# Performance work log

Measured on AMD Instinct MI355X. Metric: run time of the kernel, lower is better.

Reference implementation:

```python
import jax, jax.numpy as jnp
import numpy as np

G = 8          # grid_size
N = G * G      # 64 nodes
DEG = 17       # neighbors per node for 8x8 sudoku (2x4 boxes)
STEPS = 32
H = 96         # hidden_dim
E = 16         # embed_size
B = 16         # batch


def sudoku_edges():
    # row (7) + col (7) + 2x4 box (7) neighbors, set-union -> 17 per node
    idx = np.arange(N).reshape(G, G)
    nb = []
    for j in range(N):
        r, c = j // G, j % G
        br, bc = (r // 2) * 2, (c // 4) * 4
        s = set(idx[r, :].tolist()) | set(idx[:, c].tolist()) | set(idx[br:br + 2, bc:bc + 4].flatten().tolist())
        s.discard(j)
        nb.append(sorted(s))
    return np.asarray(nb, dtype=np.int32)  # [64, 17]


def setup_inputs() -> dict:
    key = jax.random.key(0)
    ks = jax.random.split(key, 16)
    sc = 0.05
    inp = {
        "x": jax.random.randint(ks[0], (B, G, G), 0, G + 1),            # given digits, 0 = blank
        "target": jax.random.randint(ks[1], (B, G, G), 0, G) + 1,       # solutions in 1..8
        "edges": jnp.asarray(sudoku_edges()),                            # [64, 17] int32
        "digit_emb": jax.random.normal(ks[2], (G + 1, E), jnp.float32) * sc,
        "row_emb": jax.random.normal(ks[3], (G, E), jnp.float32) * sc,
        "col_emb": jax.random.normal(ks[4], (G, E), jnp.float32) * sc,
        "in0_W": jax.random.normal(ks[5], (3 * E, H), jnp.float32) * sc,
        "in0_b": jnp.zeros((H,), jnp.float32),
        "in_Ws": jax.random.normal(ks[6], (3, H, H), jnp.float32) * sc,
        "in_bs": jnp.zeros((3, H), jnp.float32),
        "msg0_W": jax.random.normal(ks[7], (2 * H, H), jnp.float32) * sc,
        "msg0_b": jnp.zeros((H,), jnp.float32),
        "msg_Ws": jax.random.normal(ks[8], (3, H, H), jnp.float32) * sc,
        "msg_bs": jnp.zeros((3, H), jnp.float32),
        "W_ih": jax.random.normal(ks[9], (2 * H, 4 * H), jnp.float32) * sc,
        "W_hh": jax.random.normal(ks[10], (H, 4 * H), jnp.float32) * sc,
        "b_ih": jnp.zeros((4 * H,), jnp.float32),
        "b_hh": jnp.zeros((4 * H,), jnp.float32),
        "pred_W": jax.random.normal(ks[11], (H, G), jnp.float32) * sc,
        "pred_b": jnp.zeros((G,), jnp.float32),
    }
    return inp


def _mlp(z, W0, b0, Ws, bs):
    # Linear -> ReLU -> Linear -> ReLU -> Linear -> ReLU -> Linear (def_MLP)
    z = jax.nn.relu(z @ W0 + b0)
    z = jax.nn.relu(z @ Ws[0] + bs[0])
    z = jax.nn.relu(z @ Ws[1] + bs[1])
    return z @ Ws[2] + bs[2]


def reference(x, target, edges, digit_emb, row_emb, col_emb,
              in0_W, in0_b, in_Ws, in_bs,
              msg0_W, msg0_b, msg_Ws, msg_bs,
              W_ih, W_hh, b_ih, b_hh, pred_W, pred_b):
    bsz = x.shape[0]
    xf = x.reshape(bsz, N)
    tgt = target.reshape(bsz, N) - 1                      # labels 0..7

    de = digit_emb[xf]                                    # [B,64,E]
    re = row_emb[jnp.repeat(jnp.arange(G), G)]            # [64,E]
    ce = col_emb[jnp.tile(jnp.arange(G), G)]              # [64,E]
    feat = jnp.concatenate([de,
                            jnp.broadcast_to(re[None], (bsz, N, E)),
                            jnp.broadcast_to(ce[None], (bsz, N, E))], axis=-1)
    xin = _mlp(feat, in0_W, in0_b, in_Ws, in_bs)          # [B,64,H]

    h0 = jnp.zeros((bsz, N, H), jnp.float32)
    s0 = jnp.zeros((bsz * N, H), jnp.float32)

    def step(carry, _):
        h, s, loss = carry
        # gather-by-edge message passing
        h_edges = h[:, edges]                                             # [B,64,17,H]
        h_self = jnp.broadcast_to(h[:, :, None, :], (bsz, N, DEG, H))
        msg = _mlp(jnp.concatenate([h_edges, h_self], -1),
                   msg0_W, msg0_b, msg_Ws, msg_bs).sum(axis=2)            # [B,64,H]
        # LSTMCell update
        lstm_in = jnp.concatenate([msg, xin], -1).reshape(bsz * N, 2 * H)
        gates = lstm_in @ W_ih + b_ih + h.reshape(bsz * N, H) @ W_hh + b_hh
        i, f, g, o = jnp.split(gates, 4, axis=-1)
        s2 = jax.nn.sigmoid(f) * s + jax.nn.sigmoid(i) * jnp.tanh(g)
        h2 = (jax.nn.sigmoid(o) * jnp.tanh(s2)).reshape(bsz, N, H)
        # per-step prediction / loss / accuracy
        logp = jax.nn.log_softmax(h2 @ pred_W + pred_b, axis=-1)          # [B,64,8]
        pred = jnp.argmax(logp, axis=-1)
        acc = jnp.mean(jnp.all(pred == tgt, axis=1).astype(jnp.float32))
        loss_n = -jnp.sum(jnp.take_along_axis(logp, tgt[..., None], -1)) / (bsz * N)
        return (h2, s2, loss + loss_n), acc

    (h, s, loss), accs = jax.lax.scan(step, (h0, s0, jnp.float32(0.0)), None, length=STEPS)
    loss = loss / STEPS
    final_pred = jnp.argmax(h @ pred_W + pred_b, axis=-1)                 # [B,64]
    return loss, accs, final_pred
```

## Files before the change

### kernel.cpp

```cpp
#include <hip/hip_runtime.h>

#define DEG 17
#define NSTEPS 32
#define HD 96

#define WS_U0     0
#define WS_BAR    196608
#define WS_U1     196864
#define WS_XIN    393472
#define WS_GX     491776
#define WS_LOSSP  884992
#define WS_CNTP   901376

#define W1L   0
#define W2L   9216
#define MSGB  18432
#define M0B   18720
#define VBASE 18816
#define VSTR  10272
#define VZ1    0
#define VZ2    3840
#define VGX    7680
#define VGATES 8448
#define VMSGH  9216
#define VS3T   9600
#define VH2T   9792
#define VSLC   9984
#define VLGT   10176
#define VNBRI  10208
#define BARC  (VBASE + 2*VSTR)
#define SMTOT (BARC + 8)

__global__ void init_kernel(
    const int* __restrict__ x,
    const float* __restrict__ digit_emb,
    const float* __restrict__ row_emb,
    const float* __restrict__ col_emb,
    const float* __restrict__ in0_W,
    const float* __restrict__ in0_b,
    const float* __restrict__ in_Ws,
    const float* __restrict__ in_bs,
    const float* __restrict__ msg0_b,
    float* __restrict__ xin,
    float* __restrict__ u0)
{
  const int node = blockIdx.x;
  const int j = threadIdx.x;
  const int n = node & 63;
  const int r = n >> 3, c = n & 7;
  __shared__ float feat[48];
  __shared__ float za[HD];
  __shared__ float zb[HD];
  if (j < 16)      feat[j] = digit_emb[x[node]*16 + j];
  else if (j < 32) feat[j] = row_emb[r*16 + (j-16)];
  else if (j < 48) feat[j] = col_emb[c*16 + (j-32)];
  u0[node*192 + 96 + j] = msg0_b[j];
  __syncthreads();
  float a = in0_b[j];
  for (int k = 0; k < 48; ++k) a = fmaf(feat[k], in0_W[k*HD + j], a);
  za[j] = fmaxf(a, 0.f);
  __syncthreads();
  a = in_bs[j];
  for (int k = 0; k < HD; ++k) a = fmaf(za[k], in_Ws[k*HD + j], a);
  zb[j] = fmaxf(a, 0.f);
  __syncthreads();
  a = in_bs[HD + j];
  for (int k = 0; k < HD; ++k) a = fmaf(zb[k], in_Ws[9216 + k*HD + j], a);
  za[j] = fmaxf(a, 0.f);
  __syncthreads();
  a = in_bs[2*HD + j];
  for (int k = 0; k < HD; ++k) a = fmaf(za[k], in_Ws[2*9216 + k*HD + j], a);
  xin[node*HD + j] = a;
}

__global__ __launch_bounds__(384) void gx_kernel(
    const float* __restrict__ xin, const float* __restrict__ W_ih,
    const float* __restrict__ b_ih, const float* __restrict__ b_hh,
    float* __restrict__ gx)
{
  __shared__ float xs[4*HD];
  const int tid = threadIdx.x;
  const int base = blockIdx.x * 4;
  {
    const int m = tid / HD, k = tid - m*HD;
    xs[m*HD + k] = xin[(base+m)*HD + k];
  }
  __syncthreads();
  const int j = tid;
  float a0 = b_ih[j] + b_hh[j], a1 = a0, a2 = a0, a3 = a0;
  for (int k = 0; k < HD; ++k) {
    const float w = W_ih[(96+k)*384 + j];
    a0 = fmaf(xs[k], w, a0);
    a1 = fmaf(xs[HD+k], w, a1);
    a2 = fmaf(xs[2*HD+k], w, a2);
    a3 = fmaf(xs[3*HD+k], w, a3);
  }
  gx[(base+0)*384 + j] = a0;
  gx[(base+1)*384 + j] = a1;
  gx[(base+2)*384 + j] = a2;
  gx[(base+3)*384 + j] = a3;
}

__device__ __forceinline__ void vbar(int* c, int want) {
  if ((threadIdx.x & 63) == 0)
    __hip_atomic_fetch_add(c, 1, __ATOMIC_RELEASE, __HIP_MEMORY_SCOPE_WORKGROUP);
  while (__hip_atomic_load(c, __ATOMIC_ACQUIRE, __HIP_MEMORY_SCOPE_WORKGROUP) < want)
    __builtin_amdgcn_s_sleep(1);
}

__global__ __launch_bounds__(512, 1) void solve_kernel(
    const int* __restrict__ edges,
    const float* __restrict__ msg0_W, const float* __restrict__ msg0_b,
    const float* __restrict__ msg_Ws, const float* __restrict__ msg_bs,
    const float* __restrict__ W_ih, const float* __restrict__ W_hh,
    const float* __restrict__ pred_W, const float* __restrict__ pred_b,
    const int* __restrict__ target,
    const float* __restrict__ gx,
    float* __restrict__ u0, float* __restrict__ u1,
    int* bar,
    float* __restrict__ lossP, int* __restrict__ cntP,
    float* __restrict__ final_pred_out)
{
  __shared__ float sm[SMTOT];

  const int tid = threadIdx.x;
  const int vb  = tid >> 8;
  const int vt  = tid & 255;
  const int blk = blockIdx.x;
  const int bb  = blk & 15;
  const int grp = blk >> 4;
  const int base = bb*64 + grp*4;
  const int gbase = base + vb*2;

  float* const vs = sm + VBASE + vb*VSTR;
  int* const vnbri = (int*)(vs + VNBRI);
  int* const vbc = (int*)(sm + BARC) + vb;

  for (int i = tid*4; i < 9216; i += 2048) {
    *(float4*)&sm[W1L + i] = *(const float4*)&msg_Ws[i];
    *(float4*)&sm[W2L + i] = *(const float4*)&msg_Ws[9216 + i];
  }
  if (tid < 288) sm[MSGB + tid] = msg_bs[tid];
  if (tid < 96)  sm[M0B + tid]  = msg0_b[tid];
  if (tid < 2)   ((int*)(sm + BARC))[tid] = 0;
  #pragma unroll
  for (int t = 0; t < 3; ++t) {
    const int idx = t*256 + vt;
    vs[VGX + idx] = gx[gbase*384 + idx];
  }
  if (vt < 192) {
    vs[VSLC + vt] = 0.f;
    vs[VMSGH + 192 + vt] = 0.f;
  }
  if (vt < 40) {
    const int m = vt / 20, r = vt % 20;
    vnbri[vt] = (r < DEG) ? (bb*64 + edges[((grp*4 + vb*2) + m)*DEG + r])*192 : -1;
  }
  __syncthreads();

  const float* uP = u0;
  float*       uN = u1;
  int vph = 0;

  for (int st = 0; st < NSTEPS; ++st) {
    if (vt < 240) {
      const int row = vt % 40;
      const int kh  = vt / 40;
      const int m = row / 20;
      const int k0 = kh * 16;
      const int nb = vnbri[row];
      if (nb >= 0) {
        const float* ue = uP + nb + k0;
        const float* us = uP + (gbase+m)*192 + 96 + k0;
        #pragma unroll
        for (int t = 0; t < 4; ++t) {
          const float4 a = *(const float4*)(ue + 4*t);
          const float4 b = *(const float4*)(us + 4*t);
          vs[VZ1 + (k0+4*t+0)*40 + row] = fmaxf(a.x + b.x, 0.f);
          vs[VZ1 + (k0+4*t+1)*40 + row] = fmaxf(a.y + b.y, 0.f);
          vs[VZ1 + (k0+4*t+2)*40 + row] = fmaxf(a.z + b.z, 0.f);
          vs[VZ1 + (k0+4*t+3)*40 + row] = fmaxf(a.w + b.w, 0.f);
        }
      } else {
        #pragma unroll
        for (int t = 0; t < 16; ++t) vs[VZ1 + (k0+t)*40 + row] = 0.f;
      }
    } else {
      const int i = vt - 240;
      #pragma unroll
      for (int t = 0; t < 12; ++t) vs[VS3T + i*12 + t] = 0.f;
    }
    vph += 4; vbar(vbc, vph);

    if (vt < 240) {
      const int jg = vt % 24, dg = vt / 24;
      const int j4 = jg*4, d4 = dg*4;
      float acc[4][4] = {{0.f}};
      #pragma unroll 4
      for (int k = 0; k < 96; ++k) {
        const float4 z = *(const float4*)&vs[VZ1 + k*40 + d4];
        const float4 w = *(const float4*)&sm[W1L + k*96 + j4];
        const float ze[4] = {z.x, z.y, z.z, z.w};
        const float we[4] = {w.x, w.y, w.z, w.w};
        #pragma unroll
        for (int dd = 0; dd < 4; ++dd)
          #pragma unroll
          for (int jj = 0; jj < 4; ++jj)
            acc[dd][jj] = fmaf(ze[dd], we[jj], acc[dd][jj]);
      }
      #pragma unroll
      for (int jj = 0; jj < 4; ++jj) {
        const float b1 = sm[MSGB + j4 + jj];
        float4 q;
        q.x = fmaxf(acc[0][jj] + b1, 0.f);
        q.y = fmaxf(acc[1][jj] + b1, 0.f);
        q.z = fmaxf(acc[2][jj] + b1, 0.f);
        q.w = fmaxf(acc[3][jj] + b1, 0.f);
        *(float4*)&vs[VZ2 + (j4+jj)*40 + d4] = q;
      }
    }
    vph += 4; vbar(vbc, vph);

    if (vt < 240) {
      const int jg = vt % 24, dg = vt / 24;
      const int j4 = jg*4, d4 = dg*4;
      float acc[4][4] = {{0.f}};
      #pragma unroll 4
      for (int k = 0; k < 96; ++k) {
        const float4 z = *(const float4*)&vs[VZ2 + k*40 + d4];
        const float4 w = *(const float4*)&sm[W2L + k*96 + j4];
        const float ze[4] = {z.x, z.y, z.z, z.w};
        const float we[4] = {w.x, w.y, w.z, w.w};
        #pragma unroll
        for (int dd = 0; dd < 4; ++dd)
          #pragma unroll
          for (int jj = 0; jj < 4; ++jj)
            acc[dd][jj] = fmaf(ze[dd], we[jj], acc[dd][jj]);
      }
      const int nd = d4 / 20;
      const int r0 = d4 - nd*20;
      #pragma unroll
      for (int jj = 0; jj < 4; ++jj) {
        const float b2 = sm[MSGB + 96 + j4 + jj];
        float p = 0.f;
        #pragma unroll
        for (int dd = 0; dd < 4; ++dd)
          if (r0 + dd < DEG) p += fmaxf(acc[dd][jj] + b2, 0.f);
        atomicAdd(&vs[VS3T + (j4+jj)*2 + nd], p);
      }
    }
    vph += 4; vbar(vbc, vph);

    if (vt < 192) {
      const int jg = vt % 24, kq = vt / 24;
      const int j4 = jg*4, k0 = kq*12;
      const float* W3 = msg_Ws + 2*9216;
      float acc[2][4] = {{0.f}};
      #pragma unroll
      for (int kk = 0; kk < 12; ++kk) {
        const int k = k0 + kk;
        const float2 sv = *(const float2*)&vs[VS3T + k*2];
        const float4 wv = *(const float4*)&W3[k*96 + j4];
        const float se[2] = {sv.x, sv.y};
        const float we[4] = {wv.x, wv.y, wv.z, wv.w};
        #pragma unroll
        for (int m = 0; m < 2; ++m)
          #pragma unroll
          for (int jj = 0; jj < 4; ++jj)
            acc[m][jj] = fmaf(se[m], we[jj], acc[m][jj]);
      }
      #pragma unroll
      for (int m = 0; m < 2; ++m) {
        float4 q = {acc[m][0], acc[m][1], acc[m][2], acc[m][3]};
        *(float4*)&vs[VZ1 + (kq*2 + m)*96 + j4] = q;
      }
    }
    vph += 4; vbar(vbc, vph);
    if (vt < 192) {
      const int m = vt / 96, j = vt % 96;
      float v = 17.f * sm[MSGB + 192 + j];
      #pragma unroll
      for (int kq = 0; kq < 8; ++kq) v += vs[VZ1 + (kq*2 + m)*96 + j];
      vs[VMSGH + j*2 + m] = v;
    }
    vph += 4; vbar(vbc, vph);

    {
      const int jg = vt & 63, kq = vt >> 6;
      const int j6 = jg*6, k0 = kq*48;
      const float* Wb = (k0 < 96) ? (W_ih + (size_t)k0*384) : (W_hh + (size_t)(k0-96)*384);
      float acc[2][6] = {{0.f}};
      #pragma unroll 4
      for (int kk = 0; kk < 48; ++kk) {
        const float2 iv = *(const float2*)&vs[VMSGH + (k0+kk)*2];
        const float* wp = Wb + kk*384 + j6;
        const float2 wa = *(const float2*)wp;
        const float2 wb2 = *(const float2*)(wp + 2);
        const float2 wc = *(const float2*)(wp + 4);
        const float ie[2] = {iv.x, iv.y};
        const float we[6] = {wa.x, wa.y, wb2.x, wb2.y, wc.x, wc.y};
        #pragma unroll
        for (int m = 0; m < 2; ++m)
          #pragma unroll
          for (int jj = 0; jj < 6; ++jj)
            acc[m][jj] = fmaf(ie[m], we[jj], acc[m][jj]);
      }
      #pragma unroll
      for (int m = 0; m < 2; ++m) {
        float2 qa = {acc[m][0], acc[m][1]};
        float2 qb = {acc[m][2], acc[m][3]};
        float2 qc = {acc[m][4], acc[m][5]};
        *(float2*)&vs[VZ1 + (kq*2 + m)*384 + j6]     = qa;
        *(float2*)&vs[VZ1 + (kq*2 + m)*384 + j6 + 2] = qb;
        *(float2*)&vs[VZ1 + (kq*2 + m)*384 + j6 + 4] = qc;
      }
    }
    vph += 4; vbar(vbc, vph);
    {
      #pragma unroll
      for (int t = 0; t < 3; ++t) {
        const int idx = t*256 + vt;
        const int m = idx / 384, j = idx - m*384;
        float gv = vs[VGX + idx];
        #pragma unroll
        for (int kq = 0; kq < 4; ++kq) gv += vs[VZ1 + (kq*2 + m)*384 + j];
        vs[VGATES + idx] = gv;
      }
    }
    vph += 4; vbar(vbc, vph);

    if (vt < 192) {
      const int m = vt / 96, hj = vt - m*96;
      const float gi = vs[VGATES + m*384 + hj];
      const float gf = vs[VGATES + m*384 + 96 + hj];
      const float gg = vs[VGATES + m*384 + 192 + hj];
      const float go = vs[VGATES + m*384 + 288 + hj];
      const float sv = vs[VSLC + vt];
      const float ig = 1.f/(1.f + expf(-gi));
      const float fg = 1.f/(1.f + expf(-gf));
      const float cg = tanhf(gg);
      const float og = 1.f/(1.f + expf(-go));
      const float s2 = fg*sv + ig*cg;
      const float h2 = og*tanhf(s2);
      vs[VSLC + vt] = s2;
      vs[VH2T + hj*2 + m] = h2;
      vs[VMSGH + (96+hj)*2 + m] = h2;
    }
    vph += 4; vbar(vbc, vph);

    {
      const int jg = vt & 31, kq = vt >> 5;
      const int j6 = jg*6, k0 = kq*12;
      const float* Wb = (j6 < 96) ? (msg0_W + j6) : (msg0_W + 9216 + j6 - 96);
      float acc[2][6] = {{0.f}};
      #pragma unroll
      for (int kk = 0; kk < 12; ++kk) {
        const int k = k0 + kk;
        const float2 iv = *(const float2*)&vs[VH2T + k*2];
        const float* wp = Wb + k*96;
        const float2 wa = *(const float2*)wp;
        const float2 wb2 = *(const float2*)(wp + 2);
        const float2 wc = *(const float2*)(wp + 4);
        const float ie[2] = {iv.x, iv.y};
        const float we[6] = {wa.x, wa.y, wb2.x, wb2.y, wc.x, wc.y};
        #pragma unroll
        for (int m = 0; m < 2; ++m)
          #pragma unroll
          for (int jj = 0; jj < 6; ++jj)
            acc[m][jj] = fmaf(ie[m], we[jj], acc[m][jj]);
      }
      #pragma unroll
      for (int m = 0; m < 2; ++m) {
        float2 qa = {acc[m][0], acc[m][1]};
        float2 qb = {acc[m][2], acc[m][3]};
        float2 qc = {acc[m][4], acc[m][5]};
        *(float2*)&vs[VZ1 + (kq*2 + m)*192 + j6]     = qa;
        *(float2*)&vs[VZ1 + (kq*2 + m)*192 + j6 + 2] = qb;
        *(float2*)&vs[VZ1 + (kq*2 + m)*192 + j6 + 4] = qc;
      }
    }
    vph += 4; vbar(vbc, vph);
    if (vt < 192) {
      #pragma unroll
      for (int t = 0; t < 2; ++t) {
        const int idx = t*192 + vt;
        const int m = idx / 192, j = idx - m*192;
        float v = (j >= 96) ? sm[M0B + j - 96] : 0.f;
        #pragma unroll
        for (int kq = 0; kq < 8; ++kq) v += vs[VZ1 + (kq*2 + m)*192 + j];
        uN[(gbase+m)*192 + j] = v;
      }
    } else {
      const int t2 = vt - 192;
      const int m = t2 >> 5, c = (t2 >> 2) & 7, kq2 = t2 & 3;
      float p = 0.f;
      #pragma unroll
      for (int kk = 0; kk < 24; ++kk) {
        const int k = kq2*24 + kk;
        p = fmaf(vs[VH2T + k*2 + m], pred_W[k*8 + c], p);
      }
      p += __shfl_xor(p, 1);
      p += __shfl_xor(p, 2);
      if (kq2 == 0) vs[VLGT + m*8 + c] = p + pred_b[c];
    }
    vph += 4; vbar(vbc, vph);

    if (vt < 2) {
      const int m = vt;
      const int node = gbase + m;
      float mx = vs[VLGT + m*8];
      int pred = 0;
      #pragma unroll
      for (int c = 1; c < 8; ++c) {
        const float v = vs[VLGT + m*8 + c];
        if (v > mx) { mx = v; pred = c; }
      }
      float sum = 0.f;
      #pragma unroll
      for (int c = 0; c < 8; ++c) sum += expf(vs[VLGT + m*8 + c] - mx);
      const float lse = mx + logf(sum);
      const int tgt = target[node] - 1;
      vs[VLGT + 16 + m] = lse - vs[VLGT + m*8 + tgt];
      vs[VLGT + 20 + m] = (pred == tgt) ? 1.f : 0.f;
      if (st == NSTEPS-1) final_pred_out[node] = (float)pred;
      if (m == 0) {
        lossP[st*512 + bb*32 + grp*2 + vb] = vs[VLGT+16] + vs[VLGT+17];
        cntP[st*512 + bb*32 + grp*2 + vb] = (int)(vs[VLGT+20] + vs[VLGT+21]);
      }
    }

    if (st < NSTEPS-1) {
      __syncthreads();
      if (tid == 0) {
        __hip_atomic_fetch_add(&bar[bb*16], 1, __ATOMIC_RELEASE, __HIP_MEMORY_SCOPE_AGENT);
        const int want = 16*(st+1);
        while (__hip_atomic_load(&bar[bb*16], __ATOMIC_RELAXED, __HIP_MEMORY_SCOPE_AGENT) < want)
          __builtin_amdgcn_s_sleep(2);
        __threadfence();
      }
      __syncthreads();
      float* tp = (float*)uP; uP = uN; uN = tp;
    }
  }
}

__global__ void finalize_kernel(const float* __restrict__ lossP,
                                const int* __restrict__ cntP,
                                float* __restrict__ out)
{
  __shared__ float sl[32];
  const int tid = threadIdx.x;
  const int st = tid >> 3, q = tid & 7;
  float lsum = 0.f;
  for (int i = 0; i < 64; ++i) lsum += lossP[st*512 + q*64 + i];
  lsum += __shfl_xor(lsum, 1);
  lsum += __shfl_xor(lsum, 2);
  lsum += __shfl_xor(lsum, 4);
  if (q == 0) sl[st] = lsum;
  float okc = 0.f;
  #pragma unroll
  for (int t = 0; t < 2; ++t) {
    const int bbat = q + 8*t;
    int c = 0;
    for (int i = 0; i < 32; ++i) c += cntP[st*512 + bbat*32 + i];
    okc += (c == 64) ? 1.f : 0.f;
  }
  okc += __shfl_xor(okc, 1);
  okc += __shfl_xor(okc, 2);
  okc += __shfl_xor(okc, 4);
  if (q == 0) out[1 + st] = okc / 16.f;
  __syncthreads();
  if (tid == 0) {
    float tot = 0.f;
    for (int i = 0; i < 32; ++i) tot += sl[i];
    out[0] = tot / (1024.f * (float)NSTEPS);
  }
}

extern "C" void kernel_launch(void* const* d_in, const int* in_sizes, int n_in,
                              void* d_out, int out_size, void* d_ws, size_t ws_size,
                              hipStream_t stream) {
  const int*   x         = (const int*)  d_in[0];
  const int*   target    = (const int*)  d_in[1];
  const int*   edges     = (const int*)  d_in[2];
  const float* digit_emb = (const float*)d_in[3];
  const float* row_emb   = (const float*)d_in[4];
  const float* col_emb   = (const float*)d_in[5];
  const float* in0_W     = (const float*)d_in[6];
  const float* in0_b     = (const float*)d_in[7];
  const float* in_Ws     = (const float*)d_in[8];
  const float* in_bs     = (const float*)d_in[9];
  const float* msg0_W    = (const float*)d_in[10];
  const float* msg0_b    = (const float*)d_in[11];
  const float* msg_Ws    = (const float*)d_in[12];
  const float* msg_bs    = (const float*)d_in[13];
  const float* W_ih      = (const float*)d_in[14];
  const float* W_hh      = (const float*)d_in[15];
  const float* b_ih      = (const float*)d_in[16];
  const float* b_hh      = (const float*)d_in[17];
  const float* pred_W    = (const float*)d_in[18];
  const float* pred_b    = (const float*)d_in[19];

  float* ws    = (float*)d_ws;
  float* u0    = ws + WS_U0;
  int*   bar   = (int*)(ws + WS_BAR);
  float* u1    = ws + WS_U1;
  float* xin   = ws + WS_XIN;
  float* gxb   = ws + WS_GX;
  float* lossP = ws + WS_LOSSP;
  int*   cntP  = (int*)(ws + WS_CNTP);

  hipMemsetAsync(d_ws, 0, (size_t)(196608 + 256)*sizeof(float), stream);

  init_kernel<<<1024, HD, 0, stream>>>(x, digit_emb, row_emb, col_emb,
                                       in0_W, in0_b, in_Ws, in_bs,
                                       msg0_b, xin, u0);
  gx_kernel<<<256, 384, 0, stream>>>(xin, W_ih, b_ih, b_hh, gxb);

  float* outp = (float*)d_out;
  solve_kernel<<<256, 512, 0, stream>>>(
      edges, msg0_W, msg0_b, msg_Ws, msg_bs,
      W_ih, W_hh, pred_W, pred_b, target, gxb,
      u0, u1, bar, lossP, cntP, outp + 1 + NSTEPS);

  finalize_kernel<<<1, 256, 0, stream>>>(lossP, cntP, outp);
}
```

Baseline: 1.034 ms.

## Share LSTM and message-projection GEMMs across both half-blocks with 4-node weight reuse

The LSTM gate GEMM and the msg0 projection are restructured so that the whole block computes all 4 nodes together. Each weight element loaded from global memory is now reused across 4 nodes instead of 2, halving global weight traffic per step. Both 256-thread halves split the output columns and use block-wide __syncthreads instead of per-half barriers. pred_W is also cached in shared memory. In exchange there are more cross-half reductions and full-block barriers, and the loss and count partial indexing changes to one slot per block.

```diff
diff --git a/kernel.cpp b/kernel.cpp
--- a/kernel.cpp
+++ b/kernel.cpp
@@ -12,24 +12,25 @@
 #define WS_LOSSP  884992
 #define WS_CNTP   901376
 
-#define W1L   0
-#define W2L   9216
-#define MSGB  18432
-#define M0B   18720
-#define VBASE 18816
-#define VSTR  10272
+#define W1L    0
+#define W2L    9216
+#define MSGB   18432
+#define M0B    18720
+#define PRW    18816
+#define MSGH4  19584
+#define GATES4 20352
+#define H2T4   21888
+#define SLC4   22272
+#define GX4    22656
+#define LGT    24192
+#define NBRI   24224
+#define BARC   24304
+#define VBASE  24320
+#define VSTR   7888
 #define VZ1    0
 #define VZ2    3840
-#define VGX    7680
-#define VGATES 8448
-#define VMSGH  9216
-#define VS3T   9600
-#define VH2T   9792
-#define VSLC   9984
-#define VLGT   10176
-#define VNBRI  10208
-#define BARC  (VBASE + 2*VSTR)
-#define SMTOT (BARC + 8)
+#define VS3T   7680
+#define SMTOT  (VBASE + 2*VSTR)
 
 __global__ void init_kernel(
     const int* __restrict__ x,
@@ -130,10 +131,9 @@
   const int bb  = blk & 15;
   const int grp = blk >> 4;
   const int base = bb*64 + grp*4;
-  const int gbase = base + vb*2;
 
   float* const vs = sm + VBASE + vb*VSTR;
-  int* const vnbri = (int*)(vs + VNBRI);
+  int* const nbrs = (int*)(sm + NBRI);
   int* const vbc = (int*)(sm + BARC) + vb;
 
   for (int i = tid*4; i < 9216; i += 2048) {
@@ -143,18 +143,19 @@
   if (tid < 288) sm[MSGB + tid] = msg_bs[tid];
   if (tid < 96)  sm[M0B + tid]  = msg0_b[tid];
   if (tid < 2)   ((int*)(sm + BARC))[tid] = 0;
+  for (int i = tid; i < 768; i += 512) sm[PRW + i] = pred_W[i];
   #pragma unroll
   for (int t = 0; t < 3; ++t) {
-    const int idx = t*256 + vt;
-    vs[VGX + idx] = gx[gbase*384 + idx];
-  }
-  if (vt < 192) {
-    vs[VSLC + vt] = 0.f;
-    vs[VMSGH + 192 + vt] = 0.f;
-  }
-  if (vt < 40) {
-    const int m = vt / 20, r = vt % 20;
-    vnbri[vt] = (r < DEG) ? (bb*64 + edges[((grp*4 + vb*2) + m)*DEG + r])*192 : -1;
+    const int idx = t*512 + tid;
+    sm[GX4 + idx] = gx[base*384 + idx];
+  }
+  if (tid < 384) {
+    sm[SLC4 + tid] = 0.f;
+    sm[MSGH4 + 384 + tid] = 0.f;
+  }
+  if (tid < 80) {
+    const int m = tid / 20, r = tid % 20;
+    nbrs[tid] = (r < DEG) ? (bb*64 + edges[(grp*4 + m)*DEG + r])*192 : -1;
   }
   __syncthreads();
 
@@ -168,10 +169,10 @@
       const int kh  = vt / 40;
       const int m = row / 20;
       const int k0 = kh * 16;
-      const int nb = vnbri[row];
+      const int nb = nbrs[vb*40 + row];
       if (nb >= 0) {
         const float* ue = uP + nb + k0;
-        const float* us = uP + (gbase+m)*192 + 96 + k0;
+        const float* us = uP + (base + vb*2 + m)*192 + 96 + k0;
         #pragma unroll
         for (int t = 0; t < 4; ++t) {
           const float4 a = *(const float4*)(ue + 4*t);
@@ -281,151 +282,161 @@
       float v = 17.f * sm[MSGB + 192 + j];
       #pragma unroll
       for (int kq = 0; kq < 8; ++kq) v += vs[VZ1 + (kq*2 + m)*96 + j];
-      vs[VMSGH + j*2 + m] = v;
-    }
-    vph += 4; vbar(vbc, vph);
+      sm[MSGH4 + j*4 + vb*2 + m] = v;
+    }
+    __syncthreads();
 
     {
-      const int jg = vt & 63, kq = vt >> 6;
-      const int j6 = jg*6, k0 = kq*48;
-      const float* Wb = (k0 < 96) ? (W_ih + (size_t)k0*384) : (W_hh + (size_t)(k0-96)*384);
-      float acc[2][6] = {{0.f}};
+      const int jg = vt & 31, kq = vt >> 5;
+      const int j6 = vb*192 + jg*6;
+      const int jl = jg*6;
+      const int k0 = kq*24;
+      const float* Wb = (kq < 4) ? (W_ih + (size_t)k0*384 + j6)
+                                 : (W_hh + (size_t)(k0-96)*384 + j6);
+      float acc[4][6] = {{0.f}};
       #pragma unroll 4
-      for (int kk = 0; kk < 48; ++kk) {
-        const float2 iv = *(const float2*)&vs[VMSGH + (k0+kk)*2];
-        const float* wp = Wb + kk*384 + j6;
+      for (int kk = 0; kk < 24; ++kk) {
+        const float4 mv = *(const float4*)&sm[MSGH4 + (k0+kk)*4];
+        const float* wp = Wb + (size_t)kk*384;
         const float2 wa = *(const float2*)wp;
         const float2 wb2 = *(const float2*)(wp + 2);
         const float2 wc = *(const float2*)(wp + 4);
-        const float ie[2] = {iv.x, iv.y};
+        const float me[4] = {mv.x, mv.y, mv.z, mv.w};
         const float we[6] = {wa.x, wa.y, wb2.x, wb2.y, wc.x, wc.y};
         #pragma unroll
-        for (int m = 0; m < 2; ++m)
+        for (int m = 0; m < 4; ++m)
           #pragma unroll
           for (int jj = 0; jj < 6; ++jj)
-            acc[m][jj] = fmaf(ie[m], we[jj], acc[m][jj]);
-      }
-      #pragma unroll
-      for (int m = 0; m < 2; ++m) {
+            acc[m][jj] = fmaf(me[m], we[jj], acc[m][jj]);
+      }
+      #pragma unroll
+      for (int m = 0; m < 4; ++m) {
         float2 qa = {acc[m][0], acc[m][1]};
         float2 qb = {acc[m][2], acc[m][3]};
         float2 qc = {acc[m][4], acc[m][5]};
-        *(float2*)&vs[VZ1 + (kq*2 + m)*384 + j6]     = qa;
-        *(float2*)&vs[VZ1 + (kq*2 + m)*384 + j6 + 2] = qb;
-        *(float2*)&vs[VZ1 + (kq*2 + m)*384 + j6 + 4] = qc;
-      }
-    }
-    vph += 4; vbar(vbc, vph);
+        *(float2*)&vs[VZ1 + (kq*4 + m)*192 + jl]     = qa;
+        *(float2*)&vs[VZ1 + (kq*4 + m)*192 + jl + 2] = qb;
+        *(float2*)&vs[VZ1 + (kq*4 + m)*192 + jl + 4] = qc;
+      }
+    }
+    __syncthreads();
     {
       #pragma unroll
       for (int t = 0; t < 3; ++t) {
-        const int idx = t*256 + vt;
+        const int idx = t*512 + tid;
         const int m = idx / 384, j = idx - m*384;
-        float gv = vs[VGX + idx];
-        #pragma unroll
-        for (int kq = 0; kq < 4; ++kq) gv += vs[VZ1 + (kq*2 + m)*384 + j];
-        vs[VGATES + idx] = gv;
-      }
-    }
-    vph += 4; vbar(vbc, vph);
-
-    if (vt < 192) {
-      const int m = vt / 96, hj = vt - m*96;
-      const float gi = vs[VGATES + m*384 + hj];
-      const float gf = vs[VGATES + m*384 + 96 + hj];
-      const float gg = vs[VGATES + m*384 + 192 + hj];
-      const float go = vs[VGATES + m*384 + 288 + hj];
-      const float sv = vs[VSLC + vt];
+        const int vbh = (j >= 192) ? 1 : 0;
+        const int jl = j - vbh*192;
+        const float* pb = sm + VBASE + vbh*VSTR;
+        float g = sm[GX4 + idx];
+        #pragma unroll
+        for (int kq = 0; kq < 8; ++kq) g += pb[VZ1 + (kq*4 + m)*192 + jl];
+        sm[GATES4 + idx] = g;
+      }
+    }
+    __syncthreads();
+
+    if (tid < 384) {
+      const int m = tid / 96, hj = tid - m*96;
+      const float gi = sm[GATES4 + m*384 + hj];
+      const float gf = sm[GATES4 + m*384 + 96 + hj];
+      const float gg = sm[GATES4 + m*384 + 192 + hj];
+      const float go = sm[GATES4 + m*384 + 288 + hj];
+      const float sv = sm[SLC4 + tid];
       const float ig = 1.f/(1.f + expf(-gi));
       const float fg = 1.f/(1.f + expf(-gf));
       const float cg = tanhf(gg);
       const float og = 1.f/(1.f + expf(-go));
       const float s2 = fg*sv + ig*cg;
       const float h2 = og*tanhf(s2);
-      vs[VSLC + vt] = s2;
-      vs[VH2T + hj*2 + m] = h2;
-      vs[VMSGH + (96+hj)*2 + m] = h2;
-    }
-    vph += 4; vbar(vbc, vph);
+      sm[SLC4 + tid] = s2;
+      sm[H2T4 + hj*4 + m] = h2;
+      sm[MSGH4 + (96+hj)*4 + m] = h2;
+    }
+    __syncthreads();
 
     {
-      const int jg = vt & 31, kq = vt >> 5;
-      const int j6 = jg*6, k0 = kq*12;
-      const float* Wb = (j6 < 96) ? (msg0_W + j6) : (msg0_W + 9216 + j6 - 96);
-      float acc[2][6] = {{0.f}};
-      #pragma unroll
-      for (int kk = 0; kk < 12; ++kk) {
+      const int jg = vt & 15, kq = vt >> 4;
+      const int j6 = jg*6;
+      const float* Wb = (vb == 0) ? (msg0_W + j6) : (msg0_W + 9216 + j6);
+      const int k0 = kq*6;
+      float acc[4][6] = {{0.f}};
+      #pragma unroll
+      for (int kk = 0; kk < 6; ++kk) {
         const int k = k0 + kk;
-        const float2 iv = *(const float2*)&vs[VH2T + k*2];
+        const float4 hv = *(const float4*)&sm[H2T4 + k*4];
         const float* wp = Wb + k*96;
         const float2 wa = *(const float2*)wp;
         const float2 wb2 = *(const float2*)(wp + 2);
         const float2 wc = *(const float2*)(wp + 4);
-        const float ie[2] = {iv.x, iv.y};
+        const float he[4] = {hv.x, hv.y, hv.z, hv.w};
         const float we[6] = {wa.x, wa.y, wb2.x, wb2.y, wc.x, wc.y};
         #pragma unroll
-        for (int m = 0; m < 2; ++m)
+        for (int m = 0; m < 4; ++m)
           #pragma unroll
           for (int jj = 0; jj < 6; ++jj)
-            acc[m][jj] = fmaf(ie[m], we[jj], acc[m][jj]);
-      }
-      #pragma unroll
-      for (int m = 0; m < 2; ++m) {
+            acc[m][jj] = fmaf(he[m], we[jj], acc[m][jj]);
+      }
+      #pragma unroll
+      for (int m = 0; m < 4; ++m) {
         float2 qa = {acc[m][0], acc[m][1]};
         float2 qb = {acc[m][2], acc[m][3]};
         float2 qc = {acc[m][4], acc[m][5]};
-        *(float2*)&vs[VZ1 + (kq*2 + m)*192 + j6]     = qa;
-        *(float2*)&vs[VZ1 + (kq*2 + m)*192 + j6 + 2] = qb;
-        *(float2*)&vs[VZ1 + (kq*2 + m)*192 + j6 + 4] = qc;
-      }
-    }
-    vph += 4; vbar(vbc, vph);
-    if (vt < 192) {
+        *(float2*)&vs[VZ1 + (kq*4 + m)*96 + j6]     = qa;
+        *(float2*)&vs[VZ1 + (kq*4 + m)*96 + j6 + 2] = qb;
+        *(float2*)&vs[VZ1 + (kq*4 + m)*96 + j6 + 4] = qc;
+      }
+    }
+    __syncthreads();
+    if (tid < 384) {
       #pragma unroll
       for (int t = 0; t < 2; ++t) {
-        const int idx = t*192 + vt;
+        const int idx = t*384 + tid;
         const int m = idx / 192, j = idx - m*192;
-        float v = (j >= 96) ? sm[M0B + j - 96] : 0.f;
-        #pragma unroll
-        for (int kq = 0; kq < 8; ++kq) v += vs[VZ1 + (kq*2 + m)*192 + j];
-        uN[(gbase+m)*192 + j] = v;
+        const int vbh = (j >= 96) ? 1 : 0;
+        const int jl = j - vbh*96;
+        const float* pb = sm + VBASE + vbh*VSTR;
+        float v = vbh ? sm[M0B + jl] : 0.f;
+        #pragma unroll
+        for (int kq = 0; kq < 16; ++kq) v += pb[VZ1 + (kq*4 + m)*96 + jl];
+        uN[(base+m)*192 + j] = v;
       }
     } else {
-      const int t2 = vt - 192;
+      const int t2 = tid - 384;
       const int m = t2 >> 5, c = (t2 >> 2) & 7, kq2 = t2 & 3;
       float p = 0.f;
       #pragma unroll
       for (int kk = 0; kk < 24; ++kk) {
         const int k = kq2*24 + kk;
-        p = fmaf(vs[VH2T + k*2 + m], pred_W[k*8 + c], p);
+        p = fmaf(sm[H2T4 + k*4 + m], sm[PRW + k*8 + c], p);
       }
       p += __shfl_xor(p, 1);
       p += __shfl_xor(p, 2);
-      if (kq2 == 0) vs[VLGT + m*8 + c] = p + pred_b[c];
-    }
-    vph += 4; vbar(vbc, vph);
-
-    if (vt < 2) {
-      const int m = vt;
-      const int node = gbase + m;
-      float mx = vs[VLGT + m*8];
+      if (kq2 == 0) sm[LGT + m*8 + c] = p + pred_b[c];
+    }
+    __syncthreads();
+
+    if (tid < 4) {
+      const int m = tid;
+      const int node = base + m;
+      float mx = sm[LGT + m*8];
       int pred = 0;
       #pragma unroll
       for (int c = 1; c < 8; ++c) {
-        const float v = vs[VLGT + m*8 + c];
+        const float v = sm[LGT + m*8 + c];
         if (v > mx) { mx = v; pred = c; }
       }
       float sum = 0.f;
       #pragma unroll
-      for (int c = 0; c < 8; ++c) sum += expf(vs[VLGT + m*8 + c] - mx);
+      for (int c = 0; c < 8; ++c) sum += expf(sm[LGT + m*8 + c] - mx);
       const float lse = mx + logf(sum);
       const int tgt = target[node] - 1;
-      vs[VLGT + 16 + m] = lse - vs[VLGT + m*8 + tgt];
-      vs[VLGT + 20 + m] = (pred == tgt) ? 1.f : 0.f;
+      sm[LGT + 16 + m] = lse - sm[LGT + m*8 + tgt];
+      sm[LGT + 20 + m] = (pred == tgt) ? 1.f : 0.f;
       if (st == NSTEPS-1) final_pred_out[node] = (float)pred;
       if (m == 0) {
-        lossP[st*512 + bb*32 + grp*2 + vb] = vs[VLGT+16] + vs[VLGT+17];
-        cntP[st*512 + bb*32 + grp*2 + vb] = (int)(vs[VLGT+20] + vs[VLGT+21]);
+        lossP[st*256 + blk] = sm[LGT+16] + sm[LGT+17] + sm[LGT+18] + sm[LGT+19];
+        cntP[st*256 + blk] = (int)(sm[LGT+20] + sm[LGT+21] + sm[LGT+22] + sm[LGT+23]);
       }
     }
 
@@ -439,7 +450,7 @@
         __threadfence();
       }
       __syncthreads();
-      float* tp = (float*)uP; uP = uN; uN = tp;
+      const float* tp = uP; uP = uN; uN = (float*)tp;
     }
   }
 }
@@ -452,7 +463,7 @@
   const int tid = threadIdx.x;
   const int st = tid >> 3, q = tid & 7;
   float lsum = 0.f;
-  for (int i = 0; i < 64; ++i) lsum += lossP[st*512 + q*64 + i];
+  for (int i = 0; i < 32; ++i) lsum += lossP[st*256 + q*32 + i];
   lsum += __shfl_xor(lsum, 1);
   lsum += __shfl_xor(lsum, 2);
   lsum += __shfl_xor(lsum, 4);
@@ -462,7 +473,7 @@
   for (int t = 0; t < 2; ++t) {
     const int bbat = q + 8*t;
     int c = 0;
-    for (int i = 0; i < 32; ++i) c += cntP[st*512 + bbat*32 + i];
+    for (int i = 0; i < 16; ++i) c += cntP[st*256 + i*16 + bbat];
     okc += (c == 64) ? 1.f : 0.f;
   }
   okc += __shfl_xor(okc, 1);
```

After: 1.044 ms. No clear change (+1.0%).
